# Optimization experiments

Hardware: AMD Instinct MI355X
Metric: run time of the kernel (lower is better)

Reference implementation:

```python
import jax, jax.numpy as jnp
import numpy as np


def setup_inputs() -> dict:
    key = jax.random.key(0)
    k1, k2, k3, k4 = jax.random.split(key, 4)
    B, S, E, A = 4, 4096, 1024, 1024
    embedded = jax.random.normal(k1, (B, S, E), dtype=jnp.float32)
    # nn.Linear(E, A, bias=False) weights, stored as [E, A] so y = x @ W
    Wk = jax.random.normal(k2, (E, A), dtype=jnp.float32) * (E ** -0.5)
    Wq = jax.random.normal(k3, (E, A), dtype=jnp.float32) * (E ** -0.5)
    Wv = jax.random.normal(k4, (E, A), dtype=jnp.float32) * (E ** -0.5)
    return {"embedded": embedded, "Wk": Wk, "Wq": Wq, "Wv": Wv}


def reference(embedded, Wk, Wq, Wv):
    # K, Q, V projections: [B, S, A]
    K = embedded @ Wk
    Q = embedded @ Wq
    V = embedded @ Wv
    A = K.shape[-1]
    S = embedded.shape[1]
    # causal scores [B, S, S]
    scores = jnp.einsum("bqa,bka->bqk", Q, K) / jnp.sqrt(jnp.float32(A))
    causal = jnp.tril(jnp.ones((S, S), dtype=bool))
    scores = jnp.where(causal, scores, -jnp.inf)
    probs = jax.nn.softmax(scores, axis=-1)
    out = jnp.einsum("bqk,bka->bqa", probs, V)
    # torch.round(out, decimals=4)
    return jnp.round(out, 4)
```

## Files before the change

kernel.cpp:

```cpp
#include <hip/hip_runtime.h>
#include <hip/hip_fp16.h>

typedef __attribute__((ext_vector_type(4))) float f32x4;
typedef __attribute__((ext_vector_type(8))) short s16x8;
typedef __attribute__((ext_vector_type(4))) short s16x4;
typedef unsigned short u16;
typedef unsigned int u32;

__device__ __forceinline__ u16 f2bf(float f) {
    union { float f; unsigned u; } x; x.f = f;
    return (u16)((x.u + 0x7fffu + ((x.u >> 16) & 1u)) >> 16);
}

__device__ __forceinline__ void ld16(const void* g, void* l) {
    __builtin_amdgcn_global_load_lds(
        (const __attribute__((address_space(1))) unsigned int*)g,
        (__attribute__((address_space(3))) unsigned int*)l, 16, 0, 0);
}

__device__ __forceinline__ void kstep64(const u16* gA, const u16* gB, const u16* gC,
                                        long lda, long ldb,
                                        u16* sA, u16* sB,
                                        int wm, int wn, int lm, int lg,
                                        f32x4 acc0[4][4], f32x4 acc1[4][4])
{
    const int t = threadIdx.x;
    __syncthreads();
#pragma unroll
    for (int p = 0; p < 4; p++) {
        ld16(gA + (long)p * 32 * lda, sA + p * 2048 + t * 8);
        ld16(gB + (long)p * 32 * ldb, sB + p * 2048 + t * 8);
        ld16(gC + (long)p * 32 * ldb, sB + 8192 + p * 2048 + t * 8);
    }
    __syncthreads();

#pragma unroll
    for (int s = 0; s < 2; s++) {
        s16x8 af[4], bf[4], cf[4];
        const int co = (((s * 4 + lg) ^ (lm & 7)) << 3);
#pragma unroll
        for (int i = 0; i < 4; i++) {
            af[i] = *(const s16x8*)&sA[(wm + i * 16 + lm) * 64 + co];
            bf[i] = *(const s16x8*)&sB[(wn + i * 16 + lm) * 64 + co];
            cf[i] = *(const s16x8*)&sB[8192 + (wn + i * 16 + lm) * 64 + co];
        }
#pragma unroll
        for (int i = 0; i < 4; i++)
#pragma unroll
            for (int j = 0; j < 4; j++) {
                acc0[i][j] = __builtin_amdgcn_mfma_f32_16x16x32_bf16(af[i], bf[j], acc0[i][j], 0, 0, 0);
                acc1[i][j] = __builtin_amdgcn_mfma_f32_16x16x32_bf16(af[i], cf[j], acc1[i][j], 0, 0, 0);
            }
    }
}

__device__ __forceinline__ void gemm_core64(const u16* A, long lda,
                                            const u16* B0, const u16* B1, long ldb,
                                            int m0, int kEnd,
                                            f32x4 acc0[4][4], f32x4 acc1[4][4],
                                            u16* sA, u16* sB)
{
    const int t    = threadIdx.x;
    const int lane = t & 63;
    const int wave = t >> 6;
    const int wm   = (wave & 1) << 6;
    const int wn   = (wave >> 1) << 6;
    const int lm   = lane & 15;
    const int lg   = lane >> 4;
    const int sr   = t >> 3;
    const int sc   = (((t & 7) ^ ((t >> 3) & 7)) << 3);
    const u16* gA0 = A + (long)(m0 + sr) * lda + sc;
    const u16* gB0 = B0 + (long)sr * ldb + sc;
    const u16* gC0 = B1 + (long)sr * ldb + sc;

    for (int k0 = 0; k0 < kEnd; k0 += 64)
        kstep64(gA0 + k0, gB0 + k0, gC0 + k0, lda, ldb,
                sA, sB, wm, wn, lm, lg, acc0, acc1);
}

__global__ __launch_bounds__(256) void convert_all(const float* __restrict__ X,
                                                   const float* __restrict__ Wk,
                                                   const float* __restrict__ Wq,
                                                   const float* __restrict__ Wv,
                                                   u16* __restrict__ Xb,
                                                   u16* __restrict__ Wkt,
                                                   u16* __restrict__ Wqt,
                                                   u16* __restrict__ Wvt,
                                                   float* __restrict__ l) {
    __shared__ u16 tile[64][65];
    const int bid = blockIdx.x;
    const int t   = threadIdx.x;

    if (bid < 16384) {
        long idx = ((long)bid * 256 + t) * 4;
        f32x4 v = *(const f32x4*)&X[idx];
        s16x4 o;
        o.x = (short)f2bf(v.x); o.y = (short)f2bf(v.y);
        o.z = (short)f2bf(v.z); o.w = (short)f2bf(v.w);
        *(s16x4*)&Xb[idx] = o;
        return;
    }
    if (bid == 17152) {
        f32x4 z = {0.0f, 0.0f, 0.0f, 0.0f};
#pragma unroll
        for (int i = 0; i < 4; i++)
            *(f32x4*)&l[(i * 256 + t) * 4] = z;
        return;
    }
    const int wb = bid - 16384;
    const int by = wb >> 8;
    const int bxx = wb & 255;
    const float* W; u16* O;
    if (by == 0)      { W = Wk; O = Wkt; }
    else if (by == 1) { W = Wq; O = Wqt; }
    else              { W = Wv; O = Wvt; }
    int k0 = (bxx >> 4) << 6, n0 = (bxx & 15) << 6;
    int rr = t >> 4, cc = (t & 15) << 2;
#pragma unroll
    for (int i = 0; i < 4; i++) {
        int row = rr + i * 16;
        f32x4 v = *(const f32x4*)&W[(long)(k0 + row) * 1024 + n0 + cc];
        tile[row][cc + 0] = f2bf(v.x); tile[row][cc + 1] = f2bf(v.y);
        tile[row][cc + 2] = f2bf(v.z); tile[row][cc + 3] = f2bf(v.w);
    }
    __syncthreads();
#pragma unroll
    for (int i = 0; i < 4; i++) {
        int row = rr + i * 16;
        s16x4 pk;
        pk.x = (short)tile[cc + 0][row]; pk.y = (short)tile[cc + 1][row];
        pk.z = (short)tile[cc + 2][row]; pk.w = (short)tile[cc + 3][row];
        *(s16x4*)&O[(long)(n0 + row) * 1024 + k0 + cc] = pk;
    }
}

__device__ __forceinline__ void stage_half64(const u16* gbase, u16* lbase,
                                             int kt, int h, int t) {
    const u16* g = gbase + (long)(h * 128) * 1024 + kt * 64;
    u16* l = lbase + h * 8192 + t * 8;
    ld16(g, l);
    ld16(g + 64 * 1024, l + 4096);
}

__device__ __forceinline__ void read_A8(const u16* sA, int arow, int ih,
                                        int co0, int co1, s16x8 af[4][2]) {
#pragma unroll
    for (int i = 0; i < 4; i++) {
        af[i][0] = *(const s16x8*)&sA[(arow + (ih * 4 + i) * 16) * 64 + co0];
        af[i][1] = *(const s16x8*)&sA[(arow + (ih * 4 + i) * 16) * 64 + co1];
    }
}

__device__ __forceinline__ void read_B4(const u16* sB, int brow, int jp,
                                        int co0, int co1, s16x8 bf[4][2]) {
#pragma unroll
    for (int j = 2 * jp; j < 2 * jp + 2; j++) {
        bf[j][0] = *(const s16x8*)&sB[(brow + j * 16) * 64 + co0];
        bf[j][1] = *(const s16x8*)&sB[(brow + j * 16) * 64 + co1];
    }
}

__device__ __forceinline__ void mfma16q(f32x4 acc[8][4], const s16x8 af[4][2],
                                        const s16x8 bf[4][2], int ih, int jh) {
    __builtin_amdgcn_s_setprio(1);
#pragma unroll
    for (int s = 0; s < 2; s++)
#pragma unroll
        for (int i = 0; i < 4; i++)
#pragma unroll
            for (int j = 0; j < 2; j++)
                acc[ih * 4 + i][jh * 2 + j] = __builtin_amdgcn_mfma_f32_16x16x32_bf16(
                    af[i][s], bf[jh * 2 + j][s], acc[ih * 4 + i][jh * 2 + j], 0, 0, 0);
    __builtin_amdgcn_s_setprio(0);
}

#define ABAR() asm volatile("s_barrier" ::: "memory")

__device__ __forceinline__ void gemm256_8ph(const u16* Abase, const u16* Bbase,
                                            u16* lds, int t,
                                            int arow, int brow, int co0, int co1,
                                            f32x4 acc[8][4]) {
    const int sr = t >> 3;
    const int sc = ((t & 7) ^ (sr & 7)) << 3;
    const u16* Ast = Abase + (long)sr * 1024 + sc;
    const u16* Bst = Bbase + (long)sr * 1024 + sc;
    u16* sA0 = lds;
    u16* sA1 = lds + 16384;
    u16* sB0 = lds + 32768;
    u16* sB1 = lds + 49152;

    s16x8 af[4][2], bf[4][2];

    stage_half64(Bst, sB0, 0, 0, t); stage_half64(Bst, sB0, 0, 1, t);
    stage_half64(Ast, sA0, 0, 0, t); stage_half64(Ast, sA0, 0, 1, t);
    stage_half64(Bst, sB1, 1, 0, t); stage_half64(Bst, sB1, 1, 1, t);
    asm volatile("s_waitcnt vmcnt(4)" ::: "memory");
    ABAR();

#pragma unroll 1
    for (int it = 0; it < 8; it++) {
        const int  tO   = 2 * it + 1;
        const bool more = (it < 7);
        read_A8(sA0, arow, 0, co0, co1, af);
        read_B4(sB0, brow, 0, co0, co1, bf);
        stage_half64(Ast, sA1, tO, 0, t);
        mfma16q(acc, af, bf, 0, 0);
        ABAR();
        read_B4(sB0, brow, 1, co0, co1, bf);
        stage_half64(Ast, sA1, tO, 1, t);
        mfma16q(acc, af, bf, 0, 1);
        ABAR();
        read_A8(sA0, arow, 1, co0, co1, af);
        if (more) stage_half64(Bst, sB0, tO + 1, 0, t);
        mfma16q(acc, af, bf, 1, 0);
        ABAR();
        if (more) stage_half64(Bst, sB0, tO + 1, 1, t);
        mfma16q(acc, af, bf, 1, 1);
        if (more) asm volatile("s_waitcnt vmcnt(4)" ::: "memory");
        else      asm volatile("s_waitcnt vmcnt(0)" ::: "memory");
        ABAR();
        read_A8(sA1, arow, 0, co0, co1, af);
        read_B4(sB1, brow, 0, co0, co1, bf);
        if (more) stage_half64(Ast, sA0, tO + 1, 0, t);
        mfma16q(acc, af, bf, 0, 0);
        ABAR();
        read_B4(sB1, brow, 1, co0, co1, bf);
        if (more) stage_half64(Ast, sA0, tO + 1, 1, t);
        mfma16q(acc, af, bf, 0, 1);
        ABAR();
        read_A8(sA1, arow, 1, co0, co1, af);
        if (more) stage_half64(Bst, sB1, tO + 2, 0, t);
        mfma16q(acc, af, bf, 1, 0);
        ABAR();
        if (more) stage_half64(Bst, sB1, tO + 2, 1, t);
        mfma16q(acc, af, bf, 1, 1);
        if (more) asm volatile("s_waitcnt vmcnt(4)" ::: "memory");
        ABAR();
    }
}

__global__ __launch_bounds__(512, 2) void proj_all8(const u16* __restrict__ X,
                                                    const u16* __restrict__ Wqt,
                                                    const u16* __restrict__ Wkt,
                                                    const u16* __restrict__ Wvt,
                                                    u16* __restrict__ Qb,
                                                    u16* __restrict__ Kb,
                                                    u16* __restrict__ Vt) {
    __shared__ u16 lds[65536];
    const int bx  = ((blockIdx.x & 7) * 96) + (blockIdx.x >> 3);
    const int z   = bx >> 8;
    const int rem = bx & 255;
    const int m0  = (rem >> 2) << 8;
    const int n0  = (rem & 3) << 8;
    const u16* Wt = (z == 0) ? Wqt : (z == 1) ? Wkt : Wvt;

    const int t    = threadIdx.x;
    const int lane = t & 63, w = t >> 6;
    const int wr = w >> 2, wc = w & 3;
    const int lm = lane & 15, lg = lane >> 4;
    const int arow = wr * 128 + lm;
    const int brow = wc * 64 + lm;
    const int co0 = ((lg) ^ (lm & 7)) << 3;
    const int co1 = ((4 + lg) ^ (lm & 7)) << 3;

    f32x4 acc[8][4] = {};
    gemm256_8ph(X + (long)m0 * 1024, Wt + (long)n0 * 1024, lds, t,
                arow, brow, co0, co1, acc);

    if (z < 2) {
        u16* O = (z == 0) ? Qb : Kb;
#pragma unroll
        for (int i = 0; i < 8; i++)
#pragma unroll
            for (int j = 0; j < 4; j++)
#pragma unroll
                for (int r = 0; r < 4; r++) {
                    int row = m0 + wr * 128 + i * 16 + lg * 4 + r;
                    int col = n0 + wc * 64 + j * 16 + lm;
                    O[(long)row * 1024 + col] = f2bf(acc[i][j][r]);
                }
    } else {
#pragma unroll
        for (int i = 0; i < 8; i++)
#pragma unroll
            for (int j = 0; j < 4; j++) {
                int row0 = m0 + wr * 128 + i * 16 + lg * 4;
                int col  = n0 + wc * 64 + j * 16 + lm;
                int b = row0 >> 12, s = row0 & 4095;
                s16x4 p0;
                p0.x = (short)f2bf(acc[i][j][0]); p0.y = (short)f2bf(acc[i][j][1]);
                p0.z = (short)f2bf(acc[i][j][2]); p0.w = (short)f2bf(acc[i][j][3]);
                *(s16x4*)&Vt[(long)b * 4194304 + (long)col * 4096 + s] = p0;
            }
    }
}

__global__ __launch_bounds__(256, 2) void sgemm_causal(const u16* __restrict__ Q,
                                                       const u16* __restrict__ K,
                                                       u16* __restrict__ S,
                                                       float* __restrict__ l) {
    __shared__ u16 sA[8192], sB[16384];
    int b  = blockIdx.x / 272;
    int tt = blockIdx.x % 272;
    int it = (int)(2.0f * sqrtf((float)tt + 1.0f)) - 1;
    if (it > 31) it = 31;
    if (it < 0) it = 0;
    while (it < 31 && (((it + 2) * (it + 2)) >> 2) <= tt) ++it;
    while (it > 0 && (((it + 1) * (it + 1)) >> 2) > tt) --it;
    int jp  = tt - (((it + 1) * (it + 1)) >> 2);
    int jt0 = jp * 2, jt1 = jt0 + 1;
    bool valid1 = (jt1 <= it);

    const u16* A  = Q + (long)b * 4194304;
    const u16* Kp = K + (long)b * 4194304;
    f32x4 acc0[4][4] = {}, acc1[4][4] = {};
    gemm_core64(A, 1024, Kp + (long)jt0 * 131072, Kp + (long)jt1 * 131072, 1024,
                it * 128, 1024, acc0, acc1, sA, sB);

    long tribase = (long)(b * 528 + ((it * (it + 1)) >> 1));
    u16* Sp0 = S + (tribase + jt0) * 16384;
    u16* Sp1 = S + (tribase + jt1) * 16384;
    int lane = threadIdx.x & 63, wave = threadIdx.x >> 6;
    int wm = (wave & 1) << 6, wn = (wave >> 1) << 6, lm = lane & 15, lg = lane >> 4;
    const float LOG2E = 1.44269504088896f;

    float rs[4][4];
#pragma unroll
    for (int i = 0; i < 4; i++)
#pragma unroll
        for (int r = 0; r < 4; r++) rs[i][r] = 0.0f;

#pragma unroll
    for (int i = 0; i < 4; i++)
#pragma unroll
        for (int j = 0; j < 4; j++)
#pragma unroll
            for (int r = 0; r < 4; r++) {
                int ri = wm + i * 16 + lg * 4 + r;
                int cj = wn + j * 16 + lm;
                int gi = it * 128 + ri;
                float p0 = (jt0 * 128 + cj > gi) ? 0.0f
                         : exp2f((acc0[i][j][r] * 0.03125f - 16.0f) * LOG2E);
                Sp0[ri * 128 + cj] = f2bf(p0);
                rs[i][r] += p0;
                if (valid1) {
                    float p1 = (jt1 * 128 + cj > gi) ? 0.0f
                             : exp2f((acc1[i][j][r] * 0.03125f - 16.0f) * LOG2E);
                    Sp1[ri * 128 + cj] = f2bf(p1);
                    rs[i][r] += p1;
                }
            }

#pragma unroll
    for (int i = 0; i < 4; i++)
#pragma unroll
        for (int r = 0; r < 4; r++) {
            float s = rs[i][r];
            s += __shfl_xor(s, 1, 64);
            s += __shfl_xor(s, 2, 64);
            s += __shfl_xor(s, 4, 64);
            s += __shfl_xor(s, 8, 64);
            if (lm == 0)
                atomicAdd(&l[b * 4096 + it * 128 + wm + i * 16 + lg * 4 + r], s);
        }
}

__global__ __launch_bounds__(256, 2) void pv_gemm(const u16* __restrict__ P,
                                                  const u16* __restrict__ Vt,
                                                  const float* __restrict__ l,
                                                  float* __restrict__ Out) {
    __shared__ u16 sA[8192], sB[16384];
    int g  = blockIdx.x;
    int it = (g < 256) ? (31 - (g >> 4)) : ((g - 256) >> 4);
    int rem = g & 15;
    int b   = rem >> 2;
    int atp = rem & 3;

    const int t    = threadIdx.x;
    const int lane = t & 63;
    const int wave = t >> 6;
    const int wm   = (wave & 1) << 6;
    const int wn   = (wave >> 1) << 6;
    const int lm   = lane & 15;
    const int lg   = lane >> 4;
    const int sr   = t >> 3;
    const int sc   = (((t & 7) ^ ((t >> 3) & 7)) << 3);

    const u16* Pbase = P + (long)(b * 528 + ((it * (it + 1)) >> 1)) * 16384;
    const u16* gA0 = Pbase + sr * 128 + sc;
    const u16* gB0 = Vt + (long)b * 4194304 + (long)(atp * 256 + sr) * 4096 + sc;
    const u16* gC0 = gB0 + (long)128 * 4096;

    f32x4 acc0[4][4] = {}, acc1[4][4] = {};
    for (int jt = 0; jt <= it; jt++) {
        long aoff = (long)jt * 16384;
        long boff = (long)jt * 128;
#pragma unroll
        for (int kk = 0; kk < 128; kk += 64)
            kstep64(gA0 + aoff + kk, gB0 + boff + kk, gC0 + boff + kk,
                    128, 4096, sA, sB, wm, wn, lm, lg, acc0, acc1);
    }

#pragma unroll
    for (int i = 0; i < 4; i++)
#pragma unroll
        for (int r = 0; r < 4; r++) {
            int gi = it * 128 + wm + i * 16 + lg * 4 + r;
            float scale = 1.0f / l[b * 4096 + gi];
#pragma unroll
            for (int j = 0; j < 4; j++) {
                int ga = atp * 256 + wn + j * 16 + lm;
                float* o = &Out[((long)b * 4096 + gi) * 1024 + ga];
                o[0]   = acc0[i][j][r] * scale;
                o[128] = acc1[i][j][r] * scale;
            }
        }
}

extern "C" void kernel_launch(void* const* d_in, const int* in_sizes, int n_in,
                              void* d_out, int out_size, void* d_ws, size_t ws_size,
                              hipStream_t stream) {
    const float* X  = (const float*)d_in[0];
    const float* Wk = (const float*)d_in[1];
    const float* Wq = (const float*)d_in[2];
    const float* Wv = (const float*)d_in[3];
    float* Out = (float*)d_out;

    char* w = (char*)d_ws;
    u16*   Qb   = (u16*)(w);
    u16*   Kb   = (u16*)(w + 33554432);
    u16*   Vt   = (u16*)(w + 67108864);
    float* l    = (float*)(w + 100663296);
    u16*   Xb   = (u16*)(w + 100728832);
    u16*   Wqt  = (u16*)(w + 134283264);
    u16*   Wkt  = (u16*)(w + 136380416);
    u16*   Wvt  = (u16*)(w + 138477568);
    u16*   S    = (u16*)(w + 100728832);

    convert_all<<<17153, 256, 0, stream>>>(X, Wk, Wq, Wv, Xb, Wkt, Wqt, Wvt, l);
    proj_all8<<<768, 512, 0, stream>>>(Xb, Wqt, Wkt, Wvt, Qb, Kb, Vt);
    sgemm_causal<<<1088, 256, 0, stream>>>(Qb, Kb, S, l);
    pv_gemm<<<512, 256, 0, stream>>>(S, Vt, l, Out);
}
```

Baseline: 422.1 us.

## Double-buffer LDS in score and PV GEMMs with async prefetch

```diff
diff --git a/kernel.cpp b/kernel.cpp
--- a/kernel.cpp
+++ b/kernel.cpp
@@ -18,65 +18,7 @@
         (__attribute__((address_space(3))) unsigned int*)l, 16, 0, 0);
 }
 
-__device__ __forceinline__ void kstep64(const u16* gA, const u16* gB, const u16* gC,
-                                        long lda, long ldb,
-                                        u16* sA, u16* sB,
-                                        int wm, int wn, int lm, int lg,
-                                        f32x4 acc0[4][4], f32x4 acc1[4][4])
-{
-    const int t = threadIdx.x;
-    __syncthreads();
-#pragma unroll
-    for (int p = 0; p < 4; p++) {
-        ld16(gA + (long)p * 32 * lda, sA + p * 2048 + t * 8);
-        ld16(gB + (long)p * 32 * ldb, sB + p * 2048 + t * 8);
-        ld16(gC + (long)p * 32 * ldb, sB + 8192 + p * 2048 + t * 8);
-    }
-    __syncthreads();
-
-#pragma unroll
-    for (int s = 0; s < 2; s++) {
-        s16x8 af[4], bf[4], cf[4];
-        const int co = (((s * 4 + lg) ^ (lm & 7)) << 3);
-#pragma unroll
-        for (int i = 0; i < 4; i++) {
-            af[i] = *(const s16x8*)&sA[(wm + i * 16 + lm) * 64 + co];
-            bf[i] = *(const s16x8*)&sB[(wn + i * 16 + lm) * 64 + co];
-            cf[i] = *(const s16x8*)&sB[8192 + (wn + i * 16 + lm) * 64 + co];
-        }
-#pragma unroll
-        for (int i = 0; i < 4; i++)
-#pragma unroll
-            for (int j = 0; j < 4; j++) {
-                acc0[i][j] = __builtin_amdgcn_mfma_f32_16x16x32_bf16(af[i], bf[j], acc0[i][j], 0, 0, 0);
-                acc1[i][j] = __builtin_amdgcn_mfma_f32_16x16x32_bf16(af[i], cf[j], acc1[i][j], 0, 0, 0);
-            }
-    }
-}
-
-__device__ __forceinline__ void gemm_core64(const u16* A, long lda,
-                                            const u16* B0, const u16* B1, long ldb,
-                                            int m0, int kEnd,
-                                            f32x4 acc0[4][4], f32x4 acc1[4][4],
-                                            u16* sA, u16* sB)
-{
-    const int t    = threadIdx.x;
-    const int lane = t & 63;
-    const int wave = t >> 6;
-    const int wm   = (wave & 1) << 6;
-    const int wn   = (wave >> 1) << 6;
-    const int lm   = lane & 15;
-    const int lg   = lane >> 4;
-    const int sr   = t >> 3;
-    const int sc   = (((t & 7) ^ ((t >> 3) & 7)) << 3);
-    const u16* gA0 = A + (long)(m0 + sr) * lda + sc;
-    const u16* gB0 = B0 + (long)sr * ldb + sc;
-    const u16* gC0 = B1 + (long)sr * ldb + sc;
-
-    for (int k0 = 0; k0 < kEnd; k0 += 64)
-        kstep64(gA0 + k0, gB0 + k0, gC0 + k0, lda, ldb,
-                sA, sB, wm, wn, lm, lg, acc0, acc1);
-}
+#define ABAR() asm volatile("s_barrier" ::: "memory")
 
 __global__ __launch_bounds__(256) void convert_all(const float* __restrict__ X,
                                                    const float* __restrict__ Wk,
@@ -173,8 +115,6 @@
                     af[i][s], bf[jh * 2 + j][s], acc[ih * 4 + i][jh * 2 + j], 0, 0, 0);
     __builtin_amdgcn_s_setprio(0);
 }
-
-#define ABAR() asm volatile("s_barrier" ::: "memory")
 
 __device__ __forceinline__ void gemm256_8ph(const u16* Abase, const u16* Bbase,
                                             u16* lds, int t,
@@ -295,11 +235,63 @@
     }
 }
 
+__device__ __forceinline__ void kstep32_db(const u16* cA, const u16* cB,
+                                           u16* nA, u16* nB,
+                                           const u16* gA, long strA,
+                                           const u16* gB, const u16* gC, long strB,
+                                           bool more, int t,
+                                           int wm, int wn, int lm, int lg,
+                                           f32x4 acc0[4][4], f32x4 acc1[4][4])
+{
+    const int co = (lg ^ ((lm >> 1) & 3)) << 3;
+    s16x8 af[4], bf[4];
+#pragma unroll
+    for (int i = 0; i < 4; i++)
+        af[i] = *(const s16x8*)&cA[(wm + i * 16 + lm) * 32 + co];
+#pragma unroll
+    for (int j = 0; j < 4; j++)
+        bf[j] = *(const s16x8*)&cB[(wn + j * 16 + lm) * 32 + co];
+    if (more) {
+        ld16(gA,             nA + t * 8);
+        ld16(gA + 64 * strA, nA + 2048 + t * 8);
+        ld16(gB,             nB + t * 8);
+        ld16(gB + 64 * strB, nB + 2048 + t * 8);
+    }
+    __builtin_amdgcn_s_setprio(1);
+#pragma unroll
+    for (int i = 0; i < 4; i++)
+#pragma unroll
+        for (int j = 0; j < 4; j++)
+            acc0[i][j] = __builtin_amdgcn_mfma_f32_16x16x32_bf16(af[i], bf[j], acc0[i][j], 0, 0, 0);
+    __builtin_amdgcn_s_setprio(0);
+    if (more) asm volatile("s_waitcnt vmcnt(4)" ::: "memory");
+    else      asm volatile("s_waitcnt vmcnt(0)" ::: "memory");
+    ABAR();
+
+    s16x8 cf[4];
+#pragma unroll
+    for (int j = 0; j < 4; j++)
+        cf[j] = *(const s16x8*)&cB[4096 + (wn + j * 16 + lm) * 32 + co];
+    if (more) {
+        ld16(gC,             nB + 4096 + t * 8);
+        ld16(gC + 64 * strB, nB + 4096 + 2048 + t * 8);
+    }
+    __builtin_amdgcn_s_setprio(1);
+#pragma unroll
+    for (int i = 0; i < 4; i++)
+#pragma unroll
+        for (int j = 0; j < 4; j++)
+            acc1[i][j] = __builtin_amdgcn_mfma_f32_16x16x32_bf16(af[i], cf[j], acc1[i][j], 0, 0, 0);
+    __builtin_amdgcn_s_setprio(0);
+    if (more) asm volatile("s_waitcnt vmcnt(2)" ::: "memory");
+    ABAR();
+}
+
 __global__ __launch_bounds__(256, 2) void sgemm_causal(const u16* __restrict__ Q,
                                                        const u16* __restrict__ K,
                                                        u16* __restrict__ S,
                                                        float* __restrict__ l) {
-    __shared__ u16 sA[8192], sB[16384];
+    __shared__ u16 lds[24576];
     int b  = blockIdx.x / 272;
     int tt = blockIdx.x % 272;
     int it = (int)(2.0f * sqrtf((float)tt + 1.0f)) - 1;
@@ -311,71 +303,6 @@
     int jt0 = jp * 2, jt1 = jt0 + 1;
     bool valid1 = (jt1 <= it);
 
-    const u16* A  = Q + (long)b * 4194304;
-    const u16* Kp = K + (long)b * 4194304;
-    f32x4 acc0[4][4] = {}, acc1[4][4] = {};
-    gemm_core64(A, 1024, Kp + (long)jt0 * 131072, Kp + (long)jt1 * 131072, 1024,
-                it * 128, 1024, acc0, acc1, sA, sB);
-
-    long tribase = (long)(b * 528 + ((it * (it + 1)) >> 1));
-    u16* Sp0 = S + (tribase + jt0) * 16384;
-    u16* Sp1 = S + (tribase + jt1) * 16384;
-    int lane = threadIdx.x & 63, wave = threadIdx.x >> 6;
-    int wm = (wave & 1) << 6, wn = (wave >> 1) << 6, lm = lane & 15, lg = lane >> 4;
-    const float LOG2E = 1.44269504088896f;
-
-    float rs[4][4];
-#pragma unroll
-    for (int i = 0; i < 4; i++)
-#pragma unroll
-        for (int r = 0; r < 4; r++) rs[i][r] = 0.0f;
-
-#pragma unroll
-    for (int i = 0; i < 4; i++)
-#pragma unroll
-        for (int j = 0; j < 4; j++)
-#pragma unroll
-            for (int r = 0; r < 4; r++) {
-                int ri = wm + i * 16 + lg * 4 + r;
-                int cj = wn + j * 16 + lm;
-                int gi = it * 128 + ri;
-                float p0 = (jt0 * 128 + cj > gi) ? 0.0f
-                         : exp2f((acc0[i][j][r] * 0.03125f - 16.0f) * LOG2E);
-                Sp0[ri * 128 + cj] = f2bf(p0);
-                rs[i][r] += p0;
-                if (valid1) {
-                    float p1 = (jt1 * 128 + cj > gi) ? 0.0f
-                             : exp2f((acc1[i][j][r] * 0.03125f - 16.0f) * LOG2E);
-                    Sp1[ri * 128 + cj] = f2bf(p1);
-                    rs[i][r] += p1;
-                }
-            }
-
-#pragma unroll
-    for (int i = 0; i < 4; i++)
-#pragma unroll
-        for (int r = 0; r < 4; r++) {
-            float s = rs[i][r];
-            s += __shfl_xor(s, 1, 64);
-            s += __shfl_xor(s, 2, 64);
-            s += __shfl_xor(s, 4, 64);
-            s += __shfl_xor(s, 8, 64);
-            if (lm == 0)
-                atomicAdd(&l[b * 4096 + it * 128 + wm + i * 16 + lg * 4 + r], s);
-        }
-}
-
-__global__ __launch_bounds__(256, 2) void pv_gemm(const u16* __restrict__ P,
-                                                  const u16* __restrict__ Vt,
-                                                  const float* __restrict__ l,
-                                                  float* __restrict__ Out) {
-    __shared__ u16 sA[8192], sB[16384];
-    int g  = blockIdx.x;
-    int it = (g < 256) ? (31 - (g >> 4)) : ((g - 256) >> 4);
-    int rem = g & 15;
-    int b   = rem >> 2;
-    int atp = rem & 3;
-
     const int t    = threadIdx.x;
     const int lane = t & 63;
     const int wave = t >> 6;
@@ -383,36 +310,146 @@
     const int wn   = (wave >> 1) << 6;
     const int lm   = lane & 15;
     const int lg   = lane >> 4;
-    const int sr   = t >> 3;
-    const int sc   = (((t & 7) ^ ((t >> 3) & 7)) << 3);
+
+    const int rA  = t >> 2;
+    const int csw = ((t & 3) ^ ((t >> 3) & 3)) << 3;
+
+    const u16* Qp = Q + (long)b * 4194304;
+    const u16* Kp = K + (long)b * 4194304;
+    const u16* aR = Qp + (long)(it * 128 + rA) * 1024 + csw;
+    const u16* bR = Kp + (long)jt0 * 131072 + (long)rA * 1024 + csw;
+    const u16* cR = Kp + (long)jt1 * 131072 + (long)rA * 1024 + csw;
+
+    u16* cAp = lds;          u16* nApp = lds + 4096;
+    u16* cBp = lds + 8192;   u16* nBpp = lds + 16384;
+
+    ld16(aR, cAp + t * 8);        ld16(aR + 65536, cAp + 2048 + t * 8);
+    ld16(bR, cBp + t * 8);        ld16(bR + 65536, cBp + 2048 + t * 8);
+    ld16(cR, cBp + 4096 + t * 8); ld16(cR + 65536, cBp + 4096 + 2048 + t * 8);
+    asm volatile("s_waitcnt vmcnt(2)" ::: "memory");
+    ABAR();
+
+    f32x4 acc0[4][4] = {}, acc1[4][4] = {};
+#pragma unroll 1
+    for (int k = 0; k < 32; k++) {
+        const int  nk   = (k + 1) * 32;
+        const bool more = (k < 31);
+        kstep32_db(cAp, cBp, nApp, nBpp,
+                   aR + nk, 1024, bR + nk, cR + nk, 1024,
+                   more, t, wm, wn, lm, lg, acc0, acc1);
+        u16* tp = cAp; cAp = nApp; nApp = tp;
+        tp = cBp; cBp = nBpp; nBpp = tp;
+    }
+
+    long tribase = (long)(b * 528 + ((it * (it + 1)) >> 1));
+    u16* Sp0 = S + (tribase + jt0) * 16384;
+    u16* Sp1 = S + (tribase + jt1) * 16384;
+    const float LOG2E = 1.44269504088896f;
+
+    float rs[4][4];
+#pragma unroll
+    for (int i = 0; i < 4; i++)
+#pragma unroll
+        for (int r2 = 0; r2 < 4; r2++) rs[i][r2] = 0.0f;
+
+#pragma unroll
+    for (int i = 0; i < 4; i++)
+#pragma unroll
+        for (int j = 0; j < 4; j++)
+#pragma unroll
+            for (int r2 = 0; r2 < 4; r2++) {
+                int ri = wm + i * 16 + lg * 4 + r2;
+                int cj = wn + j * 16 + lm;
+                int gi = it * 128 + ri;
+                float p0 = (jt0 * 128 + cj > gi) ? 0.0f
+                         : exp2f((acc0[i][j][r2] * 0.03125f - 16.0f) * LOG2E);
+                Sp0[ri * 128 + cj] = f2bf(p0);
+                rs[i][r2] += p0;
+                if (valid1) {
+                    float p1 = (jt1 * 128 + cj > gi) ? 0.0f
+                             : exp2f((acc1[i][j][r2] * 0.03125f - 16.0f) * LOG2E);
+                    Sp1[ri * 128 + cj] = f2bf(p1);
+                    rs[i][r2] += p1;
+                }
+            }
+
+#pragma unroll
+    for (int i = 0; i < 4; i++)
+#pragma unroll
+        for (int r2 = 0; r2 < 4; r2++) {
+            float s = rs[i][r2];
+            s += __shfl_xor(s, 1, 64);
+            s += __shfl_xor(s, 2, 64);
+            s += __shfl_xor(s, 4, 64);
+            s += __shfl_xor(s, 8, 64);
+            if (lm == 0)
+                atomicAdd(&l[b * 4096 + it * 128 + wm + i * 16 + lg * 4 + r2], s);
+        }
+}
+
+__global__ __launch_bounds__(256, 2) void pv_gemm(const u16* __restrict__ P,
+                                                  const u16* __restrict__ Vt,
+                                                  const float* __restrict__ l,
+                                                  float* __restrict__ Out) {
+    __shared__ u16 lds[24576];
+    int g  = blockIdx.x;
+    int it = (g < 256) ? (31 - (g >> 4)) : ((g - 256) >> 4);
+    int rem = g & 15;
+    int b   = rem >> 2;
+    int atp = rem & 3;
+
+    const int t    = threadIdx.x;
+    const int lane = t & 63;
+    const int wave = t >> 6;
+    const int wm   = (wave & 1) << 6;
+    const int wn   = (wave >> 1) << 6;
+    const int lm   = lane & 15;
+    const int lg   = lane >> 4;
+
+    const int rA  = t >> 2;
+    const int csw = ((t & 3) ^ ((t >> 3) & 3)) << 3;
 
     const u16* Pbase = P + (long)(b * 528 + ((it * (it + 1)) >> 1)) * 16384;
-    const u16* gA0 = Pbase + sr * 128 + sc;
-    const u16* gB0 = Vt + (long)b * 4194304 + (long)(atp * 256 + sr) * 4096 + sc;
-    const u16* gC0 = gB0 + (long)128 * 4096;
+    const u16* aRb = Pbase + (long)rA * 128 + csw;
+    const u16* bRb = Vt + (long)b * 4194304 + (long)(atp * 256 + rA) * 4096 + csw;
+    const u16* cRb = bRb + (long)128 * 4096;
+
+    u16* cAp = lds;          u16* nApp = lds + 4096;
+    u16* cBp = lds + 8192;   u16* nBpp = lds + 16384;
+
+    ld16(aRb, cAp + t * 8);        ld16(aRb + 64 * 128, cAp + 2048 + t * 8);
+    ld16(bRb, cBp + t * 8);        ld16(bRb + 64 * 4096, cBp + 2048 + t * 8);
+    ld16(cRb, cBp + 4096 + t * 8); ld16(cRb + 64 * 4096, cBp + 4096 + 2048 + t * 8);
+    asm volatile("s_waitcnt vmcnt(2)" ::: "memory");
+    ABAR();
 
     f32x4 acc0[4][4] = {}, acc1[4][4] = {};
-    for (int jt = 0; jt <= it; jt++) {
-        long aoff = (long)jt * 16384;
-        long boff = (long)jt * 128;
-#pragma unroll
-        for (int kk = 0; kk < 128; kk += 64)
-            kstep64(gA0 + aoff + kk, gB0 + boff + kk, gC0 + boff + kk,
-                    128, 4096, sA, sB, wm, wn, lm, lg, acc0, acc1);
-    }
-
-#pragma unroll
-    for (int i = 0; i < 4; i++)
-#pragma unroll
-        for (int r = 0; r < 4; r++) {
-            int gi = it * 128 + wm + i * 16 + lg * 4 + r;
+    const int nT = (it + 1) * 4;
+#pragma unroll 1
+    for (int k = 0; k < nT; k++) {
+        const bool more = (k < nT - 1);
+        const int  kn   = k + 1;
+        const long aoff = (long)(kn >> 2) * 16384 + (kn & 3) * 32;
+        const long boff = (long)(kn >> 2) * 128 + (kn & 3) * 32;
+        kstep32_db(cAp, cBp, nApp, nBpp,
+                   aRb + aoff, 128, bRb + boff, cRb + boff, 4096,
+                   more, t, wm, wn, lm, lg, acc0, acc1);
+        u16* tp = cAp; cAp = nApp; nApp = tp;
+        tp = cBp; cBp = nBpp; nBpp = tp;
+    }
+
+#pragma unroll
+    for (int i = 0; i < 4; i++)
+#pragma unroll
+        for (int r2 = 0; r2 < 4; r2++) {
+            int gi = it * 128 + wm + i * 16 + lg * 4 + r2;
             float scale = 1.0f / l[b * 4096 + gi];
 #pragma unroll
             for (int j = 0; j < 4; j++) {
                 int ga = atp * 256 + wn + j * 16 + lm;
                 float* o = &Out[((long)b * 4096 + gi) * 1024 + ga];
-                o[0]   = acc0[i][j][r] * scale;
-                o[128] = acc1[i][j][r] * scale;
+                o[0]   = acc0[i][j][r2] * scale;
+                o[128] = acc1[i][j][r2] * scale;
             }
         }
 }
```

Result: no change. 418.5 us (-0.9%).

## Shrink PV GEMM tile to 128x128, double grid, and rebalance causal row scheduling

Applied to the files above, without the earlier changes.

```diff
diff --git a/kernel.cpp b/kernel.cpp
--- a/kernel.cpp
+++ b/kernel.cpp
@@ -17,6 +17,8 @@
         (const __attribute__((address_space(1))) unsigned int*)g,
         (__attribute__((address_space(3))) unsigned int*)l, 16, 0, 0);
 }
+
+#define ABAR() asm volatile("s_barrier" ::: "memory")
 
 __device__ __forceinline__ void kstep64(const u16* gA, const u16* gB, const u16* gC,
                                         long lda, long ldb,
@@ -174,8 +176,6 @@
     __builtin_amdgcn_s_setprio(0);
 }
 
-#define ABAR() asm volatile("s_barrier" ::: "memory")
-
 __device__ __forceinline__ void gemm256_8ph(const u16* Abase, const u16* Bbase,
                                             u16* lds, int t,
                                             int arow, int brow, int co0, int co1,
@@ -365,16 +365,49 @@
         }
 }
 
-__global__ __launch_bounds__(256, 2) void pv_gemm(const u16* __restrict__ P,
+__device__ __forceinline__ void kstep64_s(const u16* gA, const u16* gB,
+                                          long lda, long ldb,
+                                          u16* sA, u16* sB,
+                                          int wm, int wn, int lm, int lg,
+                                          f32x4 acc[4][4])
+{
+    const int t = threadIdx.x;
+    __syncthreads();
+#pragma unroll
+    for (int p = 0; p < 4; p++) {
+        ld16(gA + (long)p * 32 * lda, sA + p * 2048 + t * 8);
+        ld16(gB + (long)p * 32 * ldb, sB + p * 2048 + t * 8);
+    }
+    __syncthreads();
+
+#pragma unroll
+    for (int s = 0; s < 2; s++) {
+        s16x8 af[4], bf[4];
+        const int co = (((s * 4 + lg) ^ (lm & 7)) << 3);
+#pragma unroll
+        for (int i = 0; i < 4; i++) {
+            af[i] = *(const s16x8*)&sA[(wm + i * 16 + lm) * 64 + co];
+            bf[i] = *(const s16x8*)&sB[(wn + i * 16 + lm) * 64 + co];
+        }
+#pragma unroll
+        for (int i = 0; i < 4; i++)
+#pragma unroll
+            for (int j = 0; j < 4; j++)
+                acc[i][j] = __builtin_amdgcn_mfma_f32_16x16x32_bf16(af[i], bf[j], acc[i][j], 0, 0, 0);
+    }
+}
+
+__global__ __launch_bounds__(256, 4) void pv_gemm(const u16* __restrict__ P,
                                                   const u16* __restrict__ Vt,
                                                   const float* __restrict__ l,
                                                   float* __restrict__ Out) {
-    __shared__ u16 sA[8192], sB[16384];
-    int g  = blockIdx.x;
-    int it = (g < 256) ? (31 - (g >> 4)) : ((g - 256) >> 4);
-    int rem = g & 15;
-    int b   = rem >> 2;
-    int atp = rem & 3;
+    __shared__ u16 sA[8192], sB[8192];
+    const int g = blockIdx.x;
+    const int q = g >> 8, i = g & 255;
+    const int u = i >> 5;
+    const int b = (i >> 3) & 3;
+    const int atp = i & 7;
+    const int it = (q == 0) ? u : (q == 1) ? (15 - u) : (q == 2) ? (16 + u) : (31 - u);
 
     const int t    = threadIdx.x;
     const int lane = t & 63;
@@ -387,32 +420,29 @@
     const int sc   = (((t & 7) ^ ((t >> 3) & 7)) << 3);
 
     const u16* Pbase = P + (long)(b * 528 + ((it * (it + 1)) >> 1)) * 16384;
-    const u16* gA0 = Pbase + sr * 128 + sc;
-    const u16* gB0 = Vt + (long)b * 4194304 + (long)(atp * 256 + sr) * 4096 + sc;
-    const u16* gC0 = gB0 + (long)128 * 4096;
-
-    f32x4 acc0[4][4] = {}, acc1[4][4] = {};
+    const u16* gA0 = Pbase + (long)sr * 128 + sc;
+    const u16* gB0 = Vt + (long)b * 4194304 + (long)(atp * 128 + sr) * 4096 + sc;
+
+    f32x4 acc[4][4] = {};
     for (int jt = 0; jt <= it; jt++) {
-        long aoff = (long)jt * 16384;
-        long boff = (long)jt * 128;
+        const long aoff = (long)jt * 16384;
+        const long boff = (long)jt * 128;
 #pragma unroll
         for (int kk = 0; kk < 128; kk += 64)
-            kstep64(gA0 + aoff + kk, gB0 + boff + kk, gC0 + boff + kk,
-                    128, 4096, sA, sB, wm, wn, lm, lg, acc0, acc1);
-    }
-
-#pragma unroll
-    for (int i = 0; i < 4; i++)
-#pragma unroll
-        for (int r = 0; r < 4; r++) {
-            int gi = it * 128 + wm + i * 16 + lg * 4 + r;
+            kstep64_s(gA0 + aoff + kk, gB0 + boff + kk, 128, 4096,
+                      sA, sB, wm, wn, lm, lg, acc);
+    }
+
+#pragma unroll
+    for (int ii = 0; ii < 4; ii++)
+#pragma unroll
+        for (int r2 = 0; r2 < 4; r2++) {
+            int gi = it * 128 + wm + ii * 16 + lg * 4 + r2;
             float scale = 1.0f / l[b * 4096 + gi];
 #pragma unroll
             for (int j = 0; j < 4; j++) {
-                int ga = atp * 256 + wn + j * 16 + lm;
-                float* o = &Out[((long)b * 4096 + gi) * 1024 + ga];
-                o[0]   = acc0[i][j][r] * scale;
-                o[128] = acc1[i][j][r] * scale;
+                int ga = atp * 128 + wn + j * 16 + lm;
+                Out[((long)b * 4096 + gi) * 1024 + ga] = acc[ii][j][r2] * scale;
             }
         }
 }
@@ -440,5 +470,5 @@
     convert_all<<<17153, 256, 0, stream>>>(X, Wk, Wq, Wv, Xb, Wkt, Wqt, Wvt, l);
     proj_all8<<<768, 512, 0, stream>>>(Xb, Wqt, Wkt, Wvt, Qb, Kb, Vt);
     sgemm_causal<<<1088, 256, 0, stream>>>(Qb, Kb, S, l);
-    pv_gemm<<<512, 256, 0, stream>>>(S, Vt, l, Out);
-}
+    pv_gemm<<<1024, 256, 0, stream>>>(S, Vt, l, Out);
+}
```

Result: slower. 436.6 us (+3.4%).
